# Optimization experiments

Measured on AMD Instinct MI355X. Metric: run time of the kernel, lower is better.

The kernel has to match this reference:

```python
import jax, jax.numpy as jnp
import numpy as np

B, S, D, H = 4, 2048, 768, 12
DH = D // H  # 64
SCALE = float(DH)  # att_scale == 'per_head' -> dim // num_heads


def setup_inputs() -> dict:
    key = jax.random.key(0)
    ks = jax.random.split(key, 7)
    p = 1.0 / np.sqrt(D)
    return {
        "x": jax.random.normal(ks[0], (B, S, D), dtype=jnp.float32),
        "Wq": jax.random.normal(ks[1], (D, D), dtype=jnp.float32) * p,
        "bq": jax.random.normal(ks[2], (D,), dtype=jnp.float32) * p,
        "Wk": jax.random.normal(ks[3], (D, D), dtype=jnp.float32) * p,
        "bk": jax.random.normal(ks[4], (D,), dtype=jnp.float32) * p,
        "Wv": jax.random.normal(ks[5], (D, D), dtype=jnp.float32) * p,
        "bv": jax.random.normal(ks[6], (D,), dtype=jnp.float32) * p,
    }


def reference(x, Wq, bq, Wk, bk, Wv, bv):
    # torch nn.Linear: y = x @ W.T + b
    q = x @ Wq.T + bq  # [B,S,D]
    k = x @ Wk.T + bk
    v = x @ Wv.T + bv
    # split heads -> [B,H,S,DH]
    def heads(t):
        return t.reshape(B, S, H, DH).transpose(0, 2, 1, 3)
    q, k, v = heads(q), heads(k), heads(v)
    scores = jnp.einsum("bhqd,bhkd->bhqk", q, k) / jnp.sqrt(jnp.float32(SCALE))
    probs = jax.nn.softmax(scores, axis=-1)
    h = jnp.einsum("bhqk,bhkd->bhqd", probs, v)  # [B,H,S,DH]
    return h.transpose(0, 2, 1, 3).reshape(B, S, D)
```

## Files before the change

kernel.cpp:

```cpp
#include <hip/hip_runtime.h>

#define NB 4
#define NS 2048
#define ND 768
#define NH 12
#define NDH 64
#define NM (NB * NS)

typedef __attribute__((ext_vector_type(8))) _Float16 f16x8;
typedef __attribute__((ext_vector_type(4))) _Float16 f16x4;
typedef __attribute__((ext_vector_type(8))) unsigned short u16x8;
typedef __attribute__((ext_vector_type(4))) unsigned short u16x4;
typedef __attribute__((ext_vector_type(4))) float f32x4;

__device__ __forceinline__ unsigned short f2h(float f) {
    _Float16 h = (_Float16)f;
    return __builtin_bit_cast(unsigned short, h);
}
__device__ __forceinline__ f16x8 ldf16x8(const unsigned short* p) {
    return __builtin_bit_cast(f16x8, *(const u16x8*)p);
}
__device__ __forceinline__ f16x4 ldf16x4(const unsigned short* p) {
    return __builtin_bit_cast(f16x4, *(const u16x4*)p);
}
__device__ __forceinline__ void gload_lds16(const void* g, void* l) {
    __builtin_amdgcn_global_load_lds(
        (const __attribute__((address_space(1))) void*)g,
        (__attribute__((address_space(3))) void*)l, 16, 0, 0);
}

__global__ __launch_bounds__(256)
void conv_f32_to_f16(const float* __restrict__ x,
                     const float* __restrict__ wq,
                     const float* __restrict__ wk,
                     const float* __restrict__ wv,
                     unsigned short* __restrict__ dst)
{
    const int CX = (NM * ND) / 8;
    const int CW = (ND * ND) / 8;
    int c = blockIdx.x * 256 + threadIdx.x;
    const float* src;
    int base;
    if (c < CX)               { src = x;  base = 0; }
    else if (c < CX + CW)     { src = wq; base = CX; }
    else if (c < CX + 2 * CW) { src = wk; base = CX + CW; }
    else                      { src = wv; base = CX + 2 * CW; }
    const float4* p = (const float4*)&src[(size_t)(c - base) * 8];
    float4 a = p[0], b = p[1];
    u16x8 r;
    r[0] = f2h(a.x); r[1] = f2h(a.y); r[2] = f2h(a.z); r[3] = f2h(a.w);
    r[4] = f2h(b.x); r[5] = f2h(b.y); r[6] = f2h(b.z); r[7] = f2h(b.w);
    *(u16x8*)&dst[(size_t)c * 8] = r;
}

__global__ __launch_bounds__(256)
void qkv_gemm(const unsigned short* __restrict__ xh,
              const unsigned short* __restrict__ wh,
              const float* __restrict__ bq,
              const float* __restrict__ bk,
              const float* __restrict__ bv,
              unsigned short* __restrict__ qkv)
{
    const int z = blockIdx.z;
    const unsigned short* W = wh + (size_t)z * ND * ND;
    const float* bias = (z == 0) ? bq : (z == 1) ? bk : bv;
    unsigned short* out = qkv + (size_t)z * NM * ND;

    const int m0 = blockIdx.x * 128;
    const int n0 = blockIdx.y * 128;
    const int tid = threadIdx.x;
    const int lane = tid & 63, wave = tid >> 6;
    const int quad = lane >> 4, l16 = lane & 15;
    const int wm = (wave >> 1) * 64, wn = (wave & 1) * 64;

    __shared__ __align__(16) unsigned short As[128 * 32];
    __shared__ __align__(16) unsigned short Bs[128 * 32];

    const f32x4 fz = {0.f, 0.f, 0.f, 0.f};
    f32x4 acc[4][4];
#pragma unroll
    for (int i = 0; i < 4; ++i)
#pragma unroll
        for (int j = 0; j < 4; ++j) acc[i][j] = fz;

    const int lrow = lane >> 2;
    const int lcol = (lane & 3) * 8;

    for (int kt = 0; kt < ND / 32; ++kt) {
        const int k0 = kt * 32;
        __syncthreads();
#pragma unroll
        for (int i = 0; i < 2; ++i) {
            const int seg = wave * 2 + i;
            const int row = seg * 16 + lrow;
            gload_lds16(&xh[(size_t)(m0 + row) * ND + k0 + lcol], &As[seg * 512]);
            gload_lds16(&W[(size_t)(n0 + row) * ND + k0 + lcol], &Bs[seg * 512]);
        }
        __syncthreads();

        f16x8 af[4], bf_[4];
#pragma unroll
        for (int mi = 0; mi < 4; ++mi)
            af[mi] = ldf16x8(&As[(wm + mi * 16 + l16) * 32 + quad * 8]);
#pragma unroll
        for (int ni = 0; ni < 4; ++ni)
            bf_[ni] = ldf16x8(&Bs[(wn + ni * 16 + l16) * 32 + quad * 8]);
#pragma unroll
        for (int mi = 0; mi < 4; ++mi)
#pragma unroll
            for (int ni = 0; ni < 4; ++ni)
                acc[mi][ni] = __builtin_amdgcn_mfma_f32_16x16x32_f16(
                    af[mi], bf_[ni], acc[mi][ni], 0, 0, 0);
    }

#pragma unroll
    for (int ni = 0; ni < 4; ++ni) {
        const int n = n0 + wn + ni * 16 + l16;
        const float bval = bias[n];
        const int hh = n >> 6, d = n & 63;
#pragma unroll
        for (int mi = 0; mi < 4; ++mi) {
#pragma unroll
            for (int r = 0; r < 4; ++r) {
                const int m = m0 + wm + mi * 16 + quad * 4 + r;
                const int bi = m >> 11, s = m & (NS - 1);
                out[(((size_t)(bi * NH + hh)) * NS + s) * NDH + d] =
                    f2h(acc[mi][ni][r] + bval);
            }
        }
    }
}

#define ALD 72
#define KLD 136

__global__ __launch_bounds__(256)
void attn_kernel(const unsigned short* __restrict__ qh,
                 const unsigned short* __restrict__ kh,
                 const unsigned short* __restrict__ vh,
                 float* __restrict__ out)
{
    const int bh = blockIdx.y;
    const int bb = bh / NH, hh = bh % NH;
    const int tid = threadIdx.x;
    const int lane = tid & 63, wave = tid >> 6;
    const int quad = lane >> 4, l16 = lane & 15;
    const int q0 = blockIdx.x * 128 + wave * 32;

    __shared__ __align__(16) unsigned short Ks[128 * ALD];
    __shared__ __align__(16) unsigned short VTs[64 * KLD];

    const unsigned short* qb = qh + (size_t)bh * NS * NDH;
    const unsigned short* kb = kh + (size_t)bh * NS * NDH;
    const unsigned short* vb = vh + (size_t)bh * NS * NDH;

    f16x8 bq_[2][2];
#pragma unroll
    for (int qt = 0; qt < 2; ++qt)
#pragma unroll
        for (int kk = 0; kk < 2; ++kk)
            bq_[qt][kk] = ldf16x8(
                &qb[(size_t)(q0 + qt * 16 + l16) * NDH + kk * 32 + quad * 8]);

    const float c2 = 0.18033688011112042f;

    const f32x4 fz = {0.f, 0.f, 0.f, 0.f};
    f32x4 o[2][4];
    float m2[2], lsum[2];
#pragma unroll
    for (int qt = 0; qt < 2; ++qt) {
#pragma unroll
        for (int dt = 0; dt < 4; ++dt) o[qt][dt] = fz;
        m2[qt] = -__builtin_inff();
        lsum[qt] = 0.f;
    }

    const int krow = tid >> 3;
    const int kcol = (tid & 7) * 8;
    const int vpair = tid & 31;
    const int vchunk = tid >> 5;

    u16x8 kr[4], vr0[2], vr1[2];
#pragma unroll
    for (int i = 0; i < 4; ++i)
        kr[i] = *(const u16x8*)&kb[(size_t)(krow + i * 32) * NDH + kcol];
#pragma unroll
    for (int i2 = 0; i2 < 2; ++i2) {
        const int P = vpair + i2 * 32;
        vr0[i2] = *(const u16x8*)&vb[(size_t)(2 * P) * NDH + vchunk * 8];
        vr1[i2] = *(const u16x8*)&vb[(size_t)(2 * P + 1) * NDH + vchunk * 8];
    }

    for (int kt = 0; kt < NS / 128; ++kt) {
        __syncthreads();
#pragma unroll
        for (int i = 0; i < 4; ++i)
            *(u16x8*)&Ks[(krow + i * 32) * ALD + kcol] = kr[i];
#pragma unroll
        for (int i2 = 0; i2 < 2; ++i2) {
            const int P = vpair + i2 * 32;
#pragma unroll
            for (int j = 0; j < 8; ++j) {
                unsigned pk = (unsigned)vr0[i2][j] | ((unsigned)vr1[i2][j] << 16);
                *(unsigned*)&VTs[(vchunk * 8 + j) * KLD + 2 * P] = pk;
            }
        }
        if (kt + 1 < NS / 128) {
            const int kv1 = (kt + 1) * 128;
#pragma unroll
            for (int i = 0; i < 4; ++i)
                kr[i] = *(const u16x8*)&kb[(size_t)(kv1 + krow + i * 32) * NDH + kcol];
#pragma unroll
            for (int i2 = 0; i2 < 2; ++i2) {
                const int P = vpair + i2 * 32;
                vr0[i2] = *(const u16x8*)&vb[(size_t)(kv1 + 2 * P) * NDH + vchunk * 8];
                vr1[i2] = *(const u16x8*)&vb[(size_t)(kv1 + 2 * P + 1) * NDH + vchunk * 8];
            }
        }
        __syncthreads();

#pragma unroll
        for (int half = 0; half < 2; ++half) {
            const int kvb = half * 64;

            f16x8 ak[4][2];
#pragma unroll
            for (int kvt = 0; kvt < 4; ++kvt)
#pragma unroll
                for (int kk = 0; kk < 2; ++kk)
                    ak[kvt][kk] = ldf16x8(
                        &Ks[(kvb + kvt * 16 + l16) * ALD + kk * 32 + quad * 8]);

            f32x4 st[2][4];
#pragma unroll
            for (int qt = 0; qt < 2; ++qt)
#pragma unroll
                for (int kvt = 0; kvt < 4; ++kvt) {
                    st[qt][kvt] = fz;
#pragma unroll
                    for (int kk = 0; kk < 2; ++kk)
                        st[qt][kvt] = __builtin_amdgcn_mfma_f32_16x16x32_f16(
                            ak[kvt][kk], bq_[qt][kk], st[qt][kvt], 0, 0, 0);
                }

            f16x4 av[4][4];
#pragma unroll
            for (int dt = 0; dt < 4; ++dt)
#pragma unroll
                for (int kvt = 0; kvt < 4; ++kvt)
                    av[dt][kvt] = ldf16x4(
                        &VTs[(dt * 16 + l16) * KLD + kvb + kvt * 16 + quad * 4]);

#pragma unroll
            for (int qt = 0; qt < 2; ++qt) {
                float rm = st[qt][0][0];
#pragma unroll
                for (int kvt = 0; kvt < 4; ++kvt)
#pragma unroll
                    for (int r = 0; r < 4; ++r)
                        rm = fmaxf(rm, st[qt][kvt][r]);
                rm = fmaxf(rm, __shfl_xor(rm, 16, 64));
                rm = fmaxf(rm, __shfl_xor(rm, 32, 64));

                const float mn = fmaxf(m2[qt], rm * c2);
                const float al = exp2f(m2[qt] - mn);
                m2[qt] = mn;

                float p[4][4];
                float rs = 0.f;
#pragma unroll
                for (int kvt = 0; kvt < 4; ++kvt)
#pragma unroll
                    for (int r = 0; r < 4; ++r) {
                        p[kvt][r] = exp2f(fmaf(st[qt][kvt][r], c2, -mn));
                        rs += p[kvt][r];
                    }
                rs += __shfl_xor(rs, 16, 64);
                rs += __shfl_xor(rs, 32, 64);
                lsum[qt] = lsum[qt] * al + rs;

#pragma unroll
                for (int dt = 0; dt < 4; ++dt)
                    o[qt][dt] *= al;

                f16x4 pf[4];
#pragma unroll
                for (int kvt = 0; kvt < 4; ++kvt)
#pragma unroll
                    for (int r = 0; r < 4; ++r)
                        pf[kvt][r] = (_Float16)p[kvt][r];

#pragma unroll
                for (int dt = 0; dt < 4; ++dt)
#pragma unroll
                    for (int kvt = 0; kvt < 4; ++kvt)
                        o[qt][dt] = __builtin_amdgcn_mfma_f32_16x16x16f16(
                            av[dt][kvt], pf[kvt], o[qt][dt], 0, 0, 0);
            }
        }
    }

#pragma unroll
    for (int qt = 0; qt < 2; ++qt) {
        const int q = q0 + qt * 16 + l16;
        const float inv = 1.f / lsum[qt];
#pragma unroll
        for (int dt = 0; dt < 4; ++dt) {
            float4 v;
            v.x = o[qt][dt][0] * inv;
            v.y = o[qt][dt][1] * inv;
            v.z = o[qt][dt][2] * inv;
            v.w = o[qt][dt][3] * inv;
            *(float4*)&out[((size_t)(bb * NS + q)) * ND + hh * NDH + dt * 16 + quad * 4] = v;
        }
    }
}

extern "C" void kernel_launch(void* const* d_in, const int* in_sizes, int n_in,
                              void* d_out, int out_size, void* d_ws, size_t ws_size,
                              hipStream_t stream)
{
    const float* x  = (const float*)d_in[0];
    const float* Wq = (const float*)d_in[1];
    const float* bq = (const float*)d_in[2];
    const float* Wk = (const float*)d_in[3];
    const float* bk = (const float*)d_in[4];
    const float* Wv = (const float*)d_in[5];
    const float* bv = (const float*)d_in[6];

    unsigned short* ws  = (unsigned short*)d_ws;
    unsigned short* xh  = ws;
    unsigned short* wh  = xh + (size_t)NM * ND;
    unsigned short* qkv = wh + (size_t)3 * ND * ND;
    unsigned short* qhp = qkv;
    unsigned short* khp = qkv + (size_t)NM * ND;
    unsigned short* vhp = qkv + (size_t)2 * NM * ND;

    const int convBlocks = (NM * ND + 3 * ND * ND) / (8 * 256);
    conv_f32_to_f16<<<convBlocks, 256, 0, stream>>>(x, Wq, Wk, Wv, xh);

    qkv_gemm<<<dim3(NM / 128, ND / 128, 3), 256, 0, stream>>>(
        xh, wh, bq, bk, bv, qkv);

    attn_kernel<<<dim3(NS / 128, NB * NH), 256, 0, stream>>>(
        qhp, khp, vhp, (float*)d_out);
}
```

Before: 247.2 us.

## Use lazy softmax rescaling, deferred row-sum reduction, fast exp2 and MFMA priority hints

Switches the online softmax to a lazy rescale: the running max is only updated, and O and lsum only rescaled, when some lane's new scaled max exceeds the old max by more than 8, with a wave-wide vote. Defers the cross-lane row-sum shuffle reduction to the epilogue. Also uses the hardware exp2 builtin and packed round-toward-zero f16 conversion, wraps the MFMA blocks in s_setprio, and replaces per-iteration address arithmetic with incremented pointers. This cuts shuffles, exp and rescale work per tile. In exchange it allows probabilities up to 2^8 before rescaling and rounds f16 toward zero, both of which slightly change numerics.

```diff
diff --git a/kernel.cpp b/kernel.cpp
--- a/kernel.cpp
+++ b/kernel.cpp
@@ -9,6 +9,7 @@
 
 typedef __attribute__((ext_vector_type(8))) _Float16 f16x8;
 typedef __attribute__((ext_vector_type(4))) _Float16 f16x4;
+typedef __attribute__((ext_vector_type(2))) _Float16 f16x2;
 typedef __attribute__((ext_vector_type(8))) unsigned short u16x8;
 typedef __attribute__((ext_vector_type(4))) unsigned short u16x4;
 typedef __attribute__((ext_vector_type(4))) float f32x4;
@@ -27,6 +28,29 @@
     __builtin_amdgcn_global_load_lds(
         (const __attribute__((address_space(1))) void*)g,
         (__attribute__((address_space(3))) void*)l, 16, 0, 0);
+}
+
+__device__ __forceinline__ float exp2_fast(float x) {
+#if __has_builtin(__builtin_amdgcn_exp2f)
+    return __builtin_amdgcn_exp2f(x);
+#else
+    return exp2f(x);
+#endif
+}
+
+__device__ __forceinline__ f16x4 pk4(float a, float b, float c, float d) {
+#if __has_builtin(__builtin_amdgcn_cvt_pkrtz)
+    f16x2 lo = __builtin_bit_cast(f16x2, __builtin_amdgcn_cvt_pkrtz(a, b));
+    f16x2 hi = __builtin_bit_cast(f16x2, __builtin_amdgcn_cvt_pkrtz(c, d));
+    f16x4 r;
+    r[0] = lo[0]; r[1] = lo[1]; r[2] = hi[0]; r[3] = hi[1];
+    return r;
+#else
+    f16x4 r;
+    r[0] = (_Float16)a; r[1] = (_Float16)b;
+    r[2] = (_Float16)c; r[3] = (_Float16)d;
+    return r;
+#endif
 }
 
 __global__ __launch_bounds__(256)
@@ -180,18 +204,21 @@
     const int vpair = tid & 31;
     const int vchunk = tid >> 5;
 
+    const unsigned short* kp = kb + (size_t)krow * NDH + kcol;
+    const unsigned short* vp = vb + (size_t)(2 * vpair) * NDH + vchunk * 8;
+
     u16x8 kr[4], vr0[2], vr1[2];
 #pragma unroll
     for (int i = 0; i < 4; ++i)
-        kr[i] = *(const u16x8*)&kb[(size_t)(krow + i * 32) * NDH + kcol];
+        kr[i] = *(const u16x8*)(kp + i * (32 * NDH));
 #pragma unroll
     for (int i2 = 0; i2 < 2; ++i2) {
-        const int P = vpair + i2 * 32;
-        vr0[i2] = *(const u16x8*)&vb[(size_t)(2 * P) * NDH + vchunk * 8];
-        vr1[i2] = *(const u16x8*)&vb[(size_t)(2 * P + 1) * NDH + vchunk * 8];
-    }
-
-    for (int kt = 0; kt < NS / 128; ++kt) {
+        vr0[i2] = *(const u16x8*)(vp + i2 * (64 * NDH));
+        vr1[i2] = *(const u16x8*)(vp + i2 * (64 * NDH) + NDH);
+    }
+
+    const int NT = NS / 128;
+    for (int kt = 0; kt < NT; ++kt) {
         __syncthreads();
 #pragma unroll
         for (int i = 0; i < 4; ++i)
@@ -205,16 +232,16 @@
                 *(unsigned*)&VTs[(vchunk * 8 + j) * KLD + 2 * P] = pk;
             }
         }
-        if (kt + 1 < NS / 128) {
-            const int kv1 = (kt + 1) * 128;
+        kp += 128 * NDH;
+        vp += 128 * NDH;
+        if (kt + 1 < NT) {
 #pragma unroll
             for (int i = 0; i < 4; ++i)
-                kr[i] = *(const u16x8*)&kb[(size_t)(kv1 + krow + i * 32) * NDH + kcol];
+                kr[i] = *(const u16x8*)(kp + i * (32 * NDH));
 #pragma unroll
             for (int i2 = 0; i2 < 2; ++i2) {
-                const int P = vpair + i2 * 32;
-                vr0[i2] = *(const u16x8*)&vb[(size_t)(kv1 + 2 * P) * NDH + vchunk * 8];
-                vr1[i2] = *(const u16x8*)&vb[(size_t)(kv1 + 2 * P + 1) * NDH + vchunk * 8];
+                vr0[i2] = *(const u16x8*)(vp + i2 * (64 * NDH));
+                vr1[i2] = *(const u16x8*)(vp + i2 * (64 * NDH) + NDH);
             }
         }
         __syncthreads();
@@ -232,6 +259,7 @@
                         &Ks[(kvb + kvt * 16 + l16) * ALD + kk * 32 + quad * 8]);
 
             f32x4 st[2][4];
+            __builtin_amdgcn_s_setprio(1);
 #pragma unroll
             for (int qt = 0; qt < 2; ++qt)
 #pragma unroll
@@ -242,6 +270,7 @@
                         st[qt][kvt] = __builtin_amdgcn_mfma_f32_16x16x32_f16(
                             ak[kvt][kk], bq_[qt][kk], st[qt][kvt], 0, 0, 0);
                 }
+            __builtin_amdgcn_s_setprio(0);
 
             f16x4 av[4][4];
 #pragma unroll
@@ -259,43 +288,41 @@
 #pragma unroll
                     for (int r = 0; r < 4; ++r)
                         rm = fmaxf(rm, st[qt][kvt][r]);
-                rm = fmaxf(rm, __shfl_xor(rm, 16, 64));
-                rm = fmaxf(rm, __shfl_xor(rm, 32, 64));
-
-                const float mn = fmaxf(m2[qt], rm * c2);
-                const float al = exp2f(m2[qt] - mn);
-                m2[qt] = mn;
-
-                float p[4][4];
+
+                if (!__all(rm * c2 <= m2[qt] + 8.f)) {
+                    rm = fmaxf(rm, __shfl_xor(rm, 16, 64));
+                    rm = fmaxf(rm, __shfl_xor(rm, 32, 64));
+                    const float mn = fmaxf(m2[qt], rm * c2);
+                    const float al = exp2_fast(m2[qt] - mn);
+                    m2[qt] = mn;
+                    lsum[qt] *= al;
+#pragma unroll
+                    for (int dt = 0; dt < 4; ++dt)
+                        o[qt][dt] *= al;
+                }
+                const float mn = m2[qt];
+
                 float rs = 0.f;
-#pragma unroll
-                for (int kvt = 0; kvt < 4; ++kvt)
-#pragma unroll
-                    for (int r = 0; r < 4; ++r) {
-                        p[kvt][r] = exp2f(fmaf(st[qt][kvt][r], c2, -mn));
-                        rs += p[kvt][r];
-                    }
-                rs += __shfl_xor(rs, 16, 64);
-                rs += __shfl_xor(rs, 32, 64);
-                lsum[qt] = lsum[qt] * al + rs;
-
-#pragma unroll
-                for (int dt = 0; dt < 4; ++dt)
-                    o[qt][dt] *= al;
-
                 f16x4 pf[4];
 #pragma unroll
-                for (int kvt = 0; kvt < 4; ++kvt)
-#pragma unroll
-                    for (int r = 0; r < 4; ++r)
-                        pf[kvt][r] = (_Float16)p[kvt][r];
-
+                for (int kvt = 0; kvt < 4; ++kvt) {
+                    const float p0 = exp2_fast(fmaf(st[qt][kvt][0], c2, -mn));
+                    const float p1 = exp2_fast(fmaf(st[qt][kvt][1], c2, -mn));
+                    const float p2 = exp2_fast(fmaf(st[qt][kvt][2], c2, -mn));
+                    const float p3 = exp2_fast(fmaf(st[qt][kvt][3], c2, -mn));
+                    rs += (p0 + p1) + (p2 + p3);
+                    pf[kvt] = pk4(p0, p1, p2, p3);
+                }
+                lsum[qt] += rs;
+
+                __builtin_amdgcn_s_setprio(1);
 #pragma unroll
                 for (int dt = 0; dt < 4; ++dt)
 #pragma unroll
                     for (int kvt = 0; kvt < 4; ++kvt)
                         o[qt][dt] = __builtin_amdgcn_mfma_f32_16x16x16f16(
                             av[dt][kvt], pf[kvt], o[qt][dt], 0, 0, 0);
+                __builtin_amdgcn_s_setprio(0);
             }
         }
     }
@@ -303,7 +330,10 @@
 #pragma unroll
     for (int qt = 0; qt < 2; ++qt) {
         const int q = q0 + qt * 16 + l16;
-        const float inv = 1.f / lsum[qt];
+        float l = lsum[qt];
+        l += __shfl_xor(l, 16, 64);
+        l += __shfl_xor(l, 32, 64);
+        const float inv = 1.f / l;
 #pragma unroll
         for (int dt = 0; dt < 4; ++dt) {
             float4 v;
```

Result: faster. 217.3 us (-12.1%).
